# Performance work log

Measured on AMD Instinct MI355X. Metric: run time of the kernel, lower is better.

## Reference

```python
import jax, jax.numpy as jnp
import numpy as np

DIM = 2048
NUM_EXPERTS = 64
K = 2
TEMPERATURE = 1.0


def setup_inputs() -> dict:
    key = jax.random.key(0)
    kx, kw, kb = jax.random.split(key, 3)
    x = jax.random.normal(kx, (4, 4096, DIM), dtype=jnp.float32)
    # nn.Linear(dim, num_experts): weight [num_experts, dim], bias [num_experts]
    bound = 1.0 / np.sqrt(DIM)
    W = jax.random.uniform(kw, (NUM_EXPERTS, DIM), dtype=jnp.float32, minval=-bound, maxval=bound)
    b = jax.random.uniform(kb, (NUM_EXPERTS,), dtype=jnp.float32, minval=-bound, maxval=bound)
    return {"x": x, "W": W, "b": b}


def reference(x, W, b):
    # logits: (batch, seq, num_experts)
    logits = (jnp.einsum('bsd,ed->bse', x, W) + b) / TEMPERATURE
    probs = jax.nn.softmax(logits, axis=-1)
    values, indices = jax.lax.top_k(probs, K)
    return indices, values
```

## Files before the change

### kernel.cpp

```cpp
#include <hip/hip_runtime.h>
#include <math.h>

typedef _Float16 half8 __attribute__((ext_vector_type(8)));
typedef float floatx16 __attribute__((ext_vector_type(16)));

#define DIMK 2048
#define NEXP 64
#define BM 32
#define KSPLIT 4
#define KPW (DIMK / KSPLIT)
#define CHUNK 64
#define NCHUNK (KPW / CHUNK)
#define KSTEP 16
#define NKS (CHUNK / KSTEP)

__global__ void SwitchRouter_wsplit(const float* __restrict__ W, _Float16* __restrict__ ws) {
    int t = blockIdx.x * 256 + threadIdx.x;
    if (t >= NEXP * DIMK) return;
    int e = t >> 11, k = t & (DIMK - 1);
    float w = W[e * DIMK + k];
    _Float16 h0 = (_Float16)w;
    _Float16 h1 = (_Float16)(w - (float)h0);
    int kb8 = k >> 3, kj = k & 7;
    ws[(((kb8 * 2 + 0) << 9) + (e << 3) + kj)] = h0;
    ws[(((kb8 * 2 + 1) << 9) + (e << 3) + kj)] = h1;
}

__device__ __forceinline__ bool gt_pair(float v, int i, float v2, int i2) {
    return (v > v2) || (v == v2 && i < i2);
}

__device__ __forceinline__ void stage_chunk(const float* xg, float* dst, int lane) {
#pragma unroll
    for (int j = 0; j < 8; ++j) {
        int rowj = j * 4 + (lane >> 4);
        const float* src = xg + (size_t)rowj * DIMK + (((lane & 15) ^ (rowj & 15)) << 2);
        __builtin_amdgcn_global_load_lds(
            (const __attribute__((address_space(1))) void*)src,
            (__attribute__((address_space(3))) void*)(dst + j * 256),
            16, 0, 0);
    }
}

__device__ __forceinline__ half8 ldw(const _Float16* wsp, int kglob0, int half_, int et, int limb, int row) {
    int kb8 = (kglob0 >> 3) + half_;
    return *(const half8*)(wsp + (((size_t)(kb8 * 2 + limb) << 9) + (((et << 5) + row) << 3)));
}

__global__ __launch_bounds__(256, 2)
void SwitchRouter_43078521979510_kernel(const float* __restrict__ x,
                                        const _Float16* __restrict__ wsp,
                                        const float* __restrict__ bias,
                                        float* __restrict__ out, int M)
{
    __shared__ float lds[16384];

    const int t = threadIdx.x;
    const int wv = t >> 6;
    const int lane = t & 63;
    const int row = lane & 31;
    const int half_ = lane >> 5;
    const int r0 = blockIdx.x * BM;
    const int kwb = wv * KPW;

    float* atile = lds + wv * (2 * 2048);
    const float* xg0 = x + (size_t)r0 * DIMK + kwb;

    floatx16 accP0 = {}, accQ0 = {}, accP1 = {}, accQ1 = {};
    half8 w0[4], w1[4];

    stage_chunk(xg0 + 0 * CHUNK, atile + 0 * 2048, lane);
    stage_chunk(xg0 + 1 * CHUNK, atile + 1 * 2048, lane);
    {
        int kg = kwb + 0;
        w0[0] = ldw(wsp, kg, half_, 0, 0, row);
        w0[1] = ldw(wsp, kg, half_, 0, 1, row);
        w0[2] = ldw(wsp, kg, half_, 1, 0, row);
        w0[3] = ldw(wsp, kg, half_, 1, 1, row);
    }

    for (int c = 0; c < NCHUNK; ++c) {
        if (c == NCHUNK - 1) {
            asm volatile("s_waitcnt vmcnt(4)" ::: "memory");
        } else {
            asm volatile("s_waitcnt vmcnt(12)" ::: "memory");
        }
        const float* buf = atile + (c & 1) * 2048;

#pragma unroll
        for (int ks = 0; ks < NKS; ++ks) {
            const bool last = (c == NCHUNK - 1) && (ks == NKS - 1);
            if (!last) {
                int kgn = (ks == NKS - 1) ? (kwb + (c + 1) * CHUNK)
                                          : (kwb + c * CHUNK + (ks + 1) * KSTEP);
                if ((ks & 1) == 0) {
                    w1[0] = ldw(wsp, kgn, half_, 0, 0, row);
                    w1[1] = ldw(wsp, kgn, half_, 0, 1, row);
                    w1[2] = ldw(wsp, kgn, half_, 1, 0, row);
                    w1[3] = ldw(wsp, kgn, half_, 1, 1, row);
                } else {
                    w0[0] = ldw(wsp, kgn, half_, 0, 0, row);
                    w0[1] = ldw(wsp, kgn, half_, 0, 1, row);
                    w0[2] = ldw(wsp, kgn, half_, 1, 0, row);
                    w0[3] = ldw(wsp, kgn, half_, 1, 1, row);
                }
            }

            int g = ks * 4 + half_ * 2;
            int s0 = g ^ (row & 15);
            int s1 = (g + 1) ^ (row & 15);
            float4 fa = *(const float4*)&buf[row * 64 + s0 * 4];
            float4 fb = *(const float4*)&buf[row * 64 + s1 * 4];
            float f[8] = {fa.x, fa.y, fa.z, fa.w, fb.x, fb.y, fb.z, fb.w};
            half8 a0, a1;
#pragma unroll
            for (int i = 0; i < 8; ++i) {
                _Float16 h = (_Float16)f[i];
                a0[i] = h;
                a1[i] = (_Float16)(f[i] - (float)h);
            }

            const half8* wb = ((ks & 1) == 0) ? w0 : w1;
            accP0 = __builtin_amdgcn_mfma_f32_32x32x16_f16(a0, wb[0], accP0, 0, 0, 0);
            accQ0 = __builtin_amdgcn_mfma_f32_32x32x16_f16(a0, wb[1], accQ0, 0, 0, 0);
            accP1 = __builtin_amdgcn_mfma_f32_32x32x16_f16(a0, wb[2], accP1, 0, 0, 0);
            accQ1 = __builtin_amdgcn_mfma_f32_32x32x16_f16(a0, wb[3], accQ1, 0, 0, 0);
            accP0 = __builtin_amdgcn_mfma_f32_32x32x16_f16(a1, wb[1], accP0, 0, 0, 0);
            accQ0 = __builtin_amdgcn_mfma_f32_32x32x16_f16(a1, wb[0], accQ0, 0, 0, 0);
            accP1 = __builtin_amdgcn_mfma_f32_32x32x16_f16(a1, wb[3], accP1, 0, 0, 0);
            accQ1 = __builtin_amdgcn_mfma_f32_32x32x16_f16(a1, wb[2], accQ1, 0, 0, 0);
        }

        asm volatile("s_waitcnt lgkmcnt(0)" ::: "memory");
        if (c + 2 < NCHUNK) stage_chunk(xg0 + (c + 2) * CHUNK, atile + (c & 1) * 2048, lane);
    }

    __syncthreads();
    float* red = lds;
#pragma unroll
    for (int s = 0; s < 16; ++s) {
        int rowD = (s & 3) + 8 * (s >> 2) + 4 * half_;
        red[wv * 2176 + rowD * 68 + 0 * 32 + row] = accP0[s] + accQ0[s];
        red[wv * 2176 + rowD * 68 + 1 * 32 + row] = accP1[s] + accQ1[s];
    }
    __syncthreads();

    {
        const int rr = t >> 3;
        const int g8 = t & 7;
        float l[8];
#pragma unroll
        for (int j = 0; j < 8; ++j) {
            float s = 0.f;
#pragma unroll
            for (int w = 0; w < 4; ++w) s += red[w * 2176 + rr * 68 + g8 * 8 + j];
            l[j] = s + bias[g8 * 8 + j];
        }

        float v0 = l[0];
        int   i0 = 8 * g8;
        float v1 = -INFINITY;
        int   i1 = -1;
#pragma unroll
        for (int j = 1; j < 8; ++j) {
            const float lv = l[j];
            const int   e  = 8 * g8 + j;
            if (lv > v0) { v1 = v0; i1 = i0; v0 = lv; i0 = e; }
            else if (lv > v1) { v1 = lv; i1 = e; }
        }
#pragma unroll
        for (int m = 1; m <= 4; m <<= 1) {
            const float ov0 = __shfl_xor(v0, m);
            const int   oi0 = __shfl_xor(i0, m);
            const float ov1 = __shfl_xor(v1, m);
            const int   oi1 = __shfl_xor(i1, m);
            if (gt_pair(ov0, oi0, v0, i0)) {
                if (gt_pair(v0, i0, ov1, oi1)) { v1 = v0; i1 = i0; }
                else                           { v1 = ov1; i1 = oi1; }
                v0 = ov0; i0 = oi0;
            } else if (gt_pair(ov0, oi0, v1, i1)) {
                v1 = ov0; i1 = oi0;
            }
        }
        float d = 0.f;
#pragma unroll
        for (int j = 0; j < 8; ++j) d += expf(l[j] - v0);
#pragma unroll
        for (int m = 1; m <= 4; m <<= 1) d += __shfl_xor(d, m);

        if (g8 == 0) {
            const int R = r0 + rr;
            out[2 * R]     = (float)i0;
            out[2 * R + 1] = (float)i1;
            out[2 * M + 2 * R]     = 1.f / d;
            out[2 * M + 2 * R + 1] = expf(v1 - v0) / d;
        }
    }
}

extern "C" void kernel_launch(void* const* d_in, const int* in_sizes, int n_in,
                              void* d_out, int out_size, void* d_ws, size_t ws_size,
                              hipStream_t stream) {
    const float* x  = (const float*)d_in[0];
    const float* W  = (const float*)d_in[1];
    const float* b  = (const float*)d_in[2];
    float* out = (float*)d_out;
    _Float16* ws = (_Float16*)d_ws;
    const int M = in_sizes[0] / DIMK;

    SwitchRouter_wsplit<<<(NEXP * DIMK + 255) / 256, 256, 0, stream>>>(W, ws);
    SwitchRouter_43078521979510_kernel<<<M / BM, 256, 0, stream>>>(x, ws, b, out, M);
}
```

Baseline: 37.30 us.

## Switch to 16x16x32 MFMA with direct register loads and smaller row tiles

Replaces the LDS-staged 32x32x16 MFMA pipeline with 16x16x32 MFMAs that take x straight from global memory into registers, using a four-deep register prefetch. The block tile drops to 16 rows and occupancy is raised to 4 blocks per SIMD. The split-fp16 product also drops the lo*lo term, so each step issues three MFMAs instead of four. The weight pre-split layout is rewritten to match the new MFMA operand order. The aim is to cut LDS staging traffic and MFMA count and to launch more blocks. The trade-off is more weight reloads per row, since each block now covers fewer rows, and a small accuracy change from the dropped cross term.

```diff
diff --git a/kernel.cpp b/kernel.cpp
--- a/kernel.cpp
+++ b/kernel.cpp
@@ -2,17 +2,14 @@
 #include <math.h>
 
 typedef _Float16 half8 __attribute__((ext_vector_type(8)));
-typedef float floatx16 __attribute__((ext_vector_type(16)));
+typedef float f32x4 __attribute__((ext_vector_type(4)));
 
 #define DIMK 2048
 #define NEXP 64
-#define BM 32
+#define BM 16
 #define KSPLIT 4
 #define KPW (DIMK / KSPLIT)
-#define CHUNK 64
-#define NCHUNK (KPW / CHUNK)
-#define KSTEP 16
-#define NKS (CHUNK / KSTEP)
+#define NKS (KPW / 32)
 
 __global__ void SwitchRouter_wsplit(const float* __restrict__ W, _Float16* __restrict__ ws) {
     int t = blockIdx.x * 256 + threadIdx.x;
@@ -21,139 +18,92 @@
     float w = W[e * DIMK + k];
     _Float16 h0 = (_Float16)w;
     _Float16 h1 = (_Float16)(w - (float)h0);
-    int kb8 = k >> 3, kj = k & 7;
-    ws[(((kb8 * 2 + 0) << 9) + (e << 3) + kj)] = h0;
-    ws[(((kb8 * 2 + 1) << 9) + (e << 3) + kj)] = h1;
+    int kb32 = k >> 5;
+    int lane = (((k >> 3) & 3) << 4) | (e & 15);
+    int et   = e >> 4;
+    size_t base = ((size_t)(kb32 * 2 + 0) * 4 + et) * 512 + lane * 8 + (k & 7);
+    ws[base]        = h0;
+    ws[base + 2048] = h1;
 }
 
 __device__ __forceinline__ bool gt_pair(float v, int i, float v2, int i2) {
     return (v > v2) || (v == v2 && i < i2);
 }
 
-__device__ __forceinline__ void stage_chunk(const float* xg, float* dst, int lane) {
-#pragma unroll
-    for (int j = 0; j < 8; ++j) {
-        int rowj = j * 4 + (lane >> 4);
-        const float* src = xg + (size_t)rowj * DIMK + (((lane & 15) ^ (rowj & 15)) << 2);
-        __builtin_amdgcn_global_load_lds(
-            (const __attribute__((address_space(1))) void*)src,
-            (__attribute__((address_space(3))) void*)(dst + j * 256),
-            16, 0, 0);
-    }
-}
-
-__device__ __forceinline__ half8 ldw(const _Float16* wsp, int kglob0, int half_, int et, int limb, int row) {
-    int kb8 = (kglob0 >> 3) + half_;
-    return *(const half8*)(wsp + (((size_t)(kb8 * 2 + limb) << 9) + (((et << 5) + row) << 3)));
-}
-
-__global__ __launch_bounds__(256, 2)
+__global__ __launch_bounds__(256, 4)
 void SwitchRouter_43078521979510_kernel(const float* __restrict__ x,
-                                        const _Float16* __restrict__ wsp,
+                                        const _Float16* __restrict__ ws,
                                         const float* __restrict__ bias,
                                         float* __restrict__ out, int M)
 {
-    __shared__ float lds[16384];
+    __shared__ float red[KSPLIT * BM * 68];
 
-    const int t = threadIdx.x;
-    const int wv = t >> 6;
+    const int t    = threadIdx.x;
+    const int wv   = t >> 6;
     const int lane = t & 63;
-    const int row = lane & 31;
-    const int half_ = lane >> 5;
-    const int r0 = blockIdx.x * BM;
-    const int kwb = wv * KPW;
+    const int r0   = blockIdx.x * BM;
 
-    float* atile = lds + wv * (2 * 2048);
-    const float* xg0 = x + (size_t)r0 * DIMK + kwb;
+    const float* xr = x + (size_t)(r0 + (lane & 15)) * DIMK + wv * KPW + ((lane >> 4) << 3);
+    const _Float16* wp = ws + (size_t)(wv * NKS) * 4096 + lane * 8;
 
-    floatx16 accP0 = {}, accQ0 = {}, accP1 = {}, accQ1 = {};
-    half8 w0[4], w1[4];
+    f32x4 acc[4] = {};
 
-    stage_chunk(xg0 + 0 * CHUNK, atile + 0 * 2048, lane);
-    stage_chunk(xg0 + 1 * CHUNK, atile + 1 * 2048, lane);
-    {
-        int kg = kwb + 0;
-        w0[0] = ldw(wsp, kg, half_, 0, 0, row);
-        w0[1] = ldw(wsp, kg, half_, 0, 1, row);
-        w0[2] = ldw(wsp, kg, half_, 1, 0, row);
-        w0[3] = ldw(wsp, kg, half_, 1, 1, row);
+    float4 fa[4], fb[4];
+#pragma unroll
+    for (int d = 0; d < 4; ++d) {
+        fa[d] = *(const float4*)(xr + d * 32);
+        fb[d] = *(const float4*)(xr + d * 32 + 4);
     }
 
-    for (int c = 0; c < NCHUNK; ++c) {
-        if (c == NCHUNK - 1) {
-            asm volatile("s_waitcnt vmcnt(4)" ::: "memory");
-        } else {
-            asm volatile("s_waitcnt vmcnt(12)" ::: "memory");
+#pragma unroll
+    for (int ks = 0; ks < NKS; ++ks) {
+        half8 w[8];
+#pragma unroll
+        for (int q = 0; q < 8; ++q)
+            w[q] = *(const half8*)(wp + (size_t)ks * 4096 + q * 512);
+
+        const float4 va = fa[ks & 3], vb = fb[ks & 3];
+        const float f[8] = {va.x, va.y, va.z, va.w, vb.x, vb.y, vb.z, vb.w};
+        half8 a0, a1;
+#pragma unroll
+        for (int i = 0; i < 8; ++i) {
+            _Float16 h = (_Float16)f[i];
+            a0[i] = h;
+            a1[i] = (_Float16)(f[i] - (float)h);
         }
-        const float* buf = atile + (c & 1) * 2048;
 
 #pragma unroll
-        for (int ks = 0; ks < NKS; ++ks) {
-            const bool last = (c == NCHUNK - 1) && (ks == NKS - 1);
-            if (!last) {
-                int kgn = (ks == NKS - 1) ? (kwb + (c + 1) * CHUNK)
-                                          : (kwb + c * CHUNK + (ks + 1) * KSTEP);
-                if ((ks & 1) == 0) {
-                    w1[0] = ldw(wsp, kgn, half_, 0, 0, row);
-                    w1[1] = ldw(wsp, kgn, half_, 0, 1, row);
-                    w1[2] = ldw(wsp, kgn, half_, 1, 0, row);
-                    w1[3] = ldw(wsp, kgn, half_, 1, 1, row);
-                } else {
-                    w0[0] = ldw(wsp, kgn, half_, 0, 0, row);
-                    w0[1] = ldw(wsp, kgn, half_, 0, 1, row);
-                    w0[2] = ldw(wsp, kgn, half_, 1, 0, row);
-                    w0[3] = ldw(wsp, kgn, half_, 1, 1, row);
-                }
-            }
-
-            int g = ks * 4 + half_ * 2;
-            int s0 = g ^ (row & 15);
-            int s1 = (g + 1) ^ (row & 15);
-            float4 fa = *(const float4*)&buf[row * 64 + s0 * 4];
-            float4 fb = *(const float4*)&buf[row * 64 + s1 * 4];
-            float f[8] = {fa.x, fa.y, fa.z, fa.w, fb.x, fb.y, fb.z, fb.w};
-            half8 a0, a1;
-#pragma unroll
-            for (int i = 0; i < 8; ++i) {
-                _Float16 h = (_Float16)f[i];
-                a0[i] = h;
-                a1[i] = (_Float16)(f[i] - (float)h);
-            }
-
-            const half8* wb = ((ks & 1) == 0) ? w0 : w1;
-            accP0 = __builtin_amdgcn_mfma_f32_32x32x16_f16(a0, wb[0], accP0, 0, 0, 0);
-            accQ0 = __builtin_amdgcn_mfma_f32_32x32x16_f16(a0, wb[1], accQ0, 0, 0, 0);
-            accP1 = __builtin_amdgcn_mfma_f32_32x32x16_f16(a0, wb[2], accP1, 0, 0, 0);
-            accQ1 = __builtin_amdgcn_mfma_f32_32x32x16_f16(a0, wb[3], accQ1, 0, 0, 0);
-            accP0 = __builtin_amdgcn_mfma_f32_32x32x16_f16(a1, wb[1], accP0, 0, 0, 0);
-            accQ0 = __builtin_amdgcn_mfma_f32_32x32x16_f16(a1, wb[0], accQ0, 0, 0, 0);
-            accP1 = __builtin_amdgcn_mfma_f32_32x32x16_f16(a1, wb[3], accP1, 0, 0, 0);
-            accQ1 = __builtin_amdgcn_mfma_f32_32x32x16_f16(a1, wb[2], accQ1, 0, 0, 0);
+        for (int et = 0; et < 4; ++et) {
+            acc[et] = __builtin_amdgcn_mfma_f32_16x16x32_f16(a0, w[et],     acc[et], 0, 0, 0);
+            acc[et] = __builtin_amdgcn_mfma_f32_16x16x32_f16(a1, w[et],     acc[et], 0, 0, 0);
+            acc[et] = __builtin_amdgcn_mfma_f32_16x16x32_f16(a0, w[4 + et], acc[et], 0, 0, 0);
         }
 
-        asm volatile("s_waitcnt lgkmcnt(0)" ::: "memory");
-        if (c + 2 < NCHUNK) stage_chunk(xg0 + (c + 2) * CHUNK, atile + (c & 1) * 2048, lane);
+        if (ks + 4 < NKS) {
+            fa[ks & 3] = *(const float4*)(xr + (ks + 4) * 32);
+            fb[ks & 3] = *(const float4*)(xr + (ks + 4) * 32 + 4);
+        }
     }
 
-    __syncthreads();
-    float* red = lds;
 #pragma unroll
-    for (int s = 0; s < 16; ++s) {
-        int rowD = (s & 3) + 8 * (s >> 2) + 4 * half_;
-        red[wv * 2176 + rowD * 68 + 0 * 32 + row] = accP0[s] + accQ0[s];
-        red[wv * 2176 + rowD * 68 + 1 * 32 + row] = accP1[s] + accQ1[s];
-    }
+    for (int et = 0; et < 4; ++et)
+#pragma unroll
+        for (int r = 0; r < 4; ++r) {
+            const int m = ((lane >> 4) << 2) + r;
+            const int e = (et << 4) + (lane & 15);
+            red[(wv * BM + m) * 68 + e] = acc[et][r];
+        }
     __syncthreads();
 
-    {
-        const int rr = t >> 3;
-        const int g8 = t & 7;
+    if (t < BM * 8) {
+        const int row = t >> 3;
+        const int g8  = t & 7;
         float l[8];
 #pragma unroll
         for (int j = 0; j < 8; ++j) {
             float s = 0.f;
 #pragma unroll
-            for (int w = 0; w < 4; ++w) s += red[w * 2176 + rr * 68 + g8 * 8 + j];
+            for (int w2 = 0; w2 < KSPLIT; ++w2) s += red[(w2 * BM + row) * 68 + g8 * 8 + j];
             l[j] = s + bias[g8 * 8 + j];
         }
 
@@ -189,7 +139,7 @@
         for (int m = 1; m <= 4; m <<= 1) d += __shfl_xor(d, m);
 
         if (g8 == 0) {
-            const int R = r0 + rr;
+            const int R = r0 + row;
             out[2 * R]     = (float)i0;
             out[2 * R + 1] = (float)i1;
             out[2 * M + 2 * R]     = 1.f / d;
```

New measurement: 45.40 us. +21.7%, slower.

## Drop low-low split term, deepen weight prefetch, hoist LDS reads before restaging

Applied to the files above, without the earlier changes.

Cuts the split-fp16 product from four MFMAs per expert tile to three by dropping the lo*lo term, which shrinks matrix-core work by a quarter at a small accuracy cost. It also merges the accumulators into two chains, prefetches weight fragments three steps ahead through a four-slot ring, and reads the whole LDS chunk into registers before issuing the next async stage. The goal is to cut MFMA issue time and hide global and LDS latency, at the cost of more registers and serial dependent MFMA chains on each accumulator.

```diff
diff --git a/kernel.cpp b/kernel.cpp
--- a/kernel.cpp
+++ b/kernel.cpp
@@ -2,17 +2,18 @@
 #include <math.h>
 
 typedef _Float16 half8 __attribute__((ext_vector_type(8)));
-typedef float floatx16 __attribute__((ext_vector_type(16)));
+typedef float f32x16 __attribute__((ext_vector_type(16)));
 
 #define DIMK 2048
 #define NEXP 64
 #define BM 32
-#define KSPLIT 4
-#define KPW (DIMK / KSPLIT)
+#define NW 4
+#define KPW (DIMK / NW)
 #define CHUNK 64
 #define NCHUNK (KPW / CHUNK)
 #define KSTEP 16
 #define NKS (CHUNK / KSTEP)
+#define NU (NCHUNK * NKS)
 
 __global__ void SwitchRouter_wsplit(const float* __restrict__ W, _Float16* __restrict__ ws) {
     int t = blockIdx.x * 256 + threadIdx.x;
@@ -30,18 +31,6 @@
     return (v > v2) || (v == v2 && i < i2);
 }
 
-__device__ __forceinline__ void stage_chunk(const float* xg, float* dst, int lane) {
-#pragma unroll
-    for (int j = 0; j < 8; ++j) {
-        int rowj = j * 4 + (lane >> 4);
-        const float* src = xg + (size_t)rowj * DIMK + (((lane & 15) ^ (rowj & 15)) << 2);
-        __builtin_amdgcn_global_load_lds(
-            (const __attribute__((address_space(1))) void*)src,
-            (__attribute__((address_space(3))) void*)(dst + j * 256),
-            16, 0, 0);
-    }
-}
-
 __device__ __forceinline__ half8 ldw(const _Float16* wsp, int kglob0, int half_, int et, int limb, int row) {
     int kb8 = (kglob0 >> 3) + half_;
     return *(const half8*)(wsp + (((size_t)(kb8 * 2 + limb) << 9) + (((et << 5) + row) << 3)));
@@ -55,93 +44,100 @@
 {
     __shared__ float lds[16384];
 
-    const int t = threadIdx.x;
-    const int wv = t >> 6;
-    const int lane = t & 63;
-    const int row = lane & 31;
+    const int t     = threadIdx.x;
+    const int wv    = t >> 6;
+    const int lane  = t & 63;
+    const int row   = lane & 31;
     const int half_ = lane >> 5;
-    const int r0 = blockIdx.x * BM;
-    const int kwb = wv * KPW;
-
-    float* atile = lds + wv * (2 * 2048);
+    const int r0    = blockIdx.x * BM;
+    const int kwb   = wv * KPW;
+
+    float* atile = lds + wv * 4096;
     const float* xg0 = x + (size_t)r0 * DIMK + kwb;
 
-    floatx16 accP0 = {}, accQ0 = {}, accP1 = {}, accQ1 = {};
-    half8 w0[4], w1[4];
-
-    stage_chunk(xg0 + 0 * CHUNK, atile + 0 * 2048, lane);
-    stage_chunk(xg0 + 1 * CHUNK, atile + 1 * 2048, lane);
-    {
-        int kg = kwb + 0;
-        w0[0] = ldw(wsp, kg, half_, 0, 0, row);
-        w0[1] = ldw(wsp, kg, half_, 0, 1, row);
-        w0[2] = ldw(wsp, kg, half_, 1, 0, row);
-        w0[3] = ldw(wsp, kg, half_, 1, 1, row);
-    }
+#define STAGE(c)                                                                   \
+    {                                                                              \
+        float* dst = atile + ((c) & 1) * 2048;                                     \
+        _Pragma("unroll") for (int j = 0; j < 8; ++j) {                            \
+            const int rowj = j * 4 + (lane >> 4);                                  \
+            const float* src = xg0 + (size_t)rowj * DIMK + (c) * CHUNK             \
+                               + (((lane & 15) ^ (rowj & 15)) << 2);               \
+            __builtin_amdgcn_global_load_lds(                                      \
+                (const __attribute__((address_space(1))) void*)src,                \
+                (__attribute__((address_space(3))) void*)(dst + j * 256),          \
+                16, 0, 0);                                                         \
+        }                                                                          \
+    }
+
+#define LOADW(u, slot)                                                             \
+    {                                                                              \
+        const int kg = kwb + (u) * KSTEP;                                          \
+        wr[slot][0] = ldw(wsp, kg, half_, 0, 0, row);                              \
+        wr[slot][1] = ldw(wsp, kg, half_, 0, 1, row);                              \
+        wr[slot][2] = ldw(wsp, kg, half_, 1, 0, row);                              \
+        wr[slot][3] = ldw(wsp, kg, half_, 1, 1, row);                              \
+    }
+
+    half8 wr[4][4];
+    f32x16 acc[2] = {};
+
+    LOADW(0, 0);
+    LOADW(1, 1);
+    LOADW(2, 2);
+    STAGE(0);
+    STAGE(1);
 
     for (int c = 0; c < NCHUNK; ++c) {
-        if (c == NCHUNK - 1) {
-            asm volatile("s_waitcnt vmcnt(4)" ::: "memory");
-        } else {
-            asm volatile("s_waitcnt vmcnt(12)" ::: "memory");
-        }
+        if (c == 0)              { asm volatile("s_waitcnt vmcnt(8)"  ::: "memory"); }
+        else if (c == NCHUNK-1) { asm volatile("s_waitcnt vmcnt(0)"  ::: "memory"); }
+        else                     { asm volatile("s_waitcnt vmcnt(20)" ::: "memory"); }
+
         const float* buf = atile + (c & 1) * 2048;
 
+        float4 fA[NKS], fB[NKS];
 #pragma unroll
         for (int ks = 0; ks < NKS; ++ks) {
-            const bool last = (c == NCHUNK - 1) && (ks == NKS - 1);
-            if (!last) {
-                int kgn = (ks == NKS - 1) ? (kwb + (c + 1) * CHUNK)
-                                          : (kwb + c * CHUNK + (ks + 1) * KSTEP);
-                if ((ks & 1) == 0) {
-                    w1[0] = ldw(wsp, kgn, half_, 0, 0, row);
-                    w1[1] = ldw(wsp, kgn, half_, 0, 1, row);
-                    w1[2] = ldw(wsp, kgn, half_, 1, 0, row);
-                    w1[3] = ldw(wsp, kgn, half_, 1, 1, row);
-                } else {
-                    w0[0] = ldw(wsp, kgn, half_, 0, 0, row);
-                    w0[1] = ldw(wsp, kgn, half_, 0, 1, row);
-                    w0[2] = ldw(wsp, kgn, half_, 1, 0, row);
-                    w0[3] = ldw(wsp, kgn, half_, 1, 1, row);
-                }
+            const int g  = ks * 4 + half_ * 2;
+            const int s0 = g ^ (row & 15);
+            const int s1 = (g + 1) ^ (row & 15);
+            fA[ks] = *(const float4*)&buf[row * 64 + s0 * 4];
+            fB[ks] = *(const float4*)&buf[row * 64 + s1 * 4];
+        }
+        asm volatile("s_waitcnt lgkmcnt(0)" ::: "memory");
+        if (c + 2 < NCHUNK) STAGE(c + 2);
+
+#pragma unroll
+        for (int ks = 0; ks < NKS; ++ks) {
+            const int u = c * NKS + ks;
+            if (u + 3 < NU) LOADW(u + 3, (ks + 3) & 3);
+
+            const float4 va = fA[ks], vb = fB[ks];
+            const float f[8] = {va.x, va.y, va.z, va.w, vb.x, vb.y, vb.z, vb.w};
+            half8 a0, a1;
+#pragma unroll
+            for (int j = 0; j < 8; ++j) {
+                _Float16 h = (_Float16)f[j];
+                a0[j] = h;
+                a1[j] = (_Float16)(f[j] - (float)h);
             }
 
-            int g = ks * 4 + half_ * 2;
-            int s0 = g ^ (row & 15);
-            int s1 = (g + 1) ^ (row & 15);
-            float4 fa = *(const float4*)&buf[row * 64 + s0 * 4];
-            float4 fb = *(const float4*)&buf[row * 64 + s1 * 4];
-            float f[8] = {fa.x, fa.y, fa.z, fa.w, fb.x, fb.y, fb.z, fb.w};
-            half8 a0, a1;
-#pragma unroll
-            for (int i = 0; i < 8; ++i) {
-                _Float16 h = (_Float16)f[i];
-                a0[i] = h;
-                a1[i] = (_Float16)(f[i] - (float)h);
-            }
-
-            const half8* wb = ((ks & 1) == 0) ? w0 : w1;
-            accP0 = __builtin_amdgcn_mfma_f32_32x32x16_f16(a0, wb[0], accP0, 0, 0, 0);
-            accQ0 = __builtin_amdgcn_mfma_f32_32x32x16_f16(a0, wb[1], accQ0, 0, 0, 0);
-            accP1 = __builtin_amdgcn_mfma_f32_32x32x16_f16(a0, wb[2], accP1, 0, 0, 0);
-            accQ1 = __builtin_amdgcn_mfma_f32_32x32x16_f16(a0, wb[3], accQ1, 0, 0, 0);
-            accP0 = __builtin_amdgcn_mfma_f32_32x32x16_f16(a1, wb[1], accP0, 0, 0, 0);
-            accQ0 = __builtin_amdgcn_mfma_f32_32x32x16_f16(a1, wb[0], accQ0, 0, 0, 0);
-            accP1 = __builtin_amdgcn_mfma_f32_32x32x16_f16(a1, wb[3], accP1, 0, 0, 0);
-            accQ1 = __builtin_amdgcn_mfma_f32_32x32x16_f16(a1, wb[2], accQ1, 0, 0, 0);
-        }
-
-        asm volatile("s_waitcnt lgkmcnt(0)" ::: "memory");
-        if (c + 2 < NCHUNK) stage_chunk(xg0 + (c + 2) * CHUNK, atile + (c & 1) * 2048, lane);
+            const half8* w = wr[ks];
+            acc[0] = __builtin_amdgcn_mfma_f32_32x32x16_f16(a0, w[0], acc[0], 0, 0, 0);
+            acc[0] = __builtin_amdgcn_mfma_f32_32x32x16_f16(a1, w[0], acc[0], 0, 0, 0);
+            acc[0] = __builtin_amdgcn_mfma_f32_32x32x16_f16(a0, w[1], acc[0], 0, 0, 0);
+            acc[1] = __builtin_amdgcn_mfma_f32_32x32x16_f16(a0, w[2], acc[1], 0, 0, 0);
+            acc[1] = __builtin_amdgcn_mfma_f32_32x32x16_f16(a1, w[2], acc[1], 0, 0, 0);
+            acc[1] = __builtin_amdgcn_mfma_f32_32x32x16_f16(a0, w[3], acc[1], 0, 0, 0);
+        }
     }
 
     __syncthreads();
     float* red = lds;
 #pragma unroll
     for (int s = 0; s < 16; ++s) {
-        int rowD = (s & 3) + 8 * (s >> 2) + 4 * half_;
-        red[wv * 2176 + rowD * 68 + 0 * 32 + row] = accP0[s] + accQ0[s];
-        red[wv * 2176 + rowD * 68 + 1 * 32 + row] = accP1[s] + accQ1[s];
+        const int rowD = (s & 3) + 8 * (s >> 2) + 4 * half_;
+        red[wv * 2176 + rowD * 68 + 0 * 32 + row] = acc[0][s];
+        red[wv * 2176 + rowD * 68 + 1 * 32 + row] = acc[1][s];
     }
     __syncthreads();
 
@@ -153,7 +149,7 @@
         for (int j = 0; j < 8; ++j) {
             float s = 0.f;
 #pragma unroll
-            for (int w = 0; w < 4; ++w) s += red[w * 2176 + rr * 68 + g8 * 8 + j];
+            for (int w2 = 0; w2 < NW; ++w2) s += red[w2 * 2176 + rr * 68 + g8 * 8 + j];
             l[j] = s + bias[g8 * 8 + j];
         }
 
@@ -169,11 +165,11 @@
             else if (lv > v1) { v1 = lv; i1 = e; }
         }
 #pragma unroll
-        for (int m = 1; m <= 4; m <<= 1) {
-            const float ov0 = __shfl_xor(v0, m);
-            const int   oi0 = __shfl_xor(i0, m);
-            const float ov1 = __shfl_xor(v1, m);
-            const int   oi1 = __shfl_xor(i1, m);
+        for (int m2 = 1; m2 <= 4; m2 <<= 1) {
+            const float ov0 = __shfl_xor(v0, m2);
+            const int   oi0 = __shfl_xor(i0, m2);
+            const float ov1 = __shfl_xor(v1, m2);
+            const int   oi1 = __shfl_xor(i1, m2);
             if (gt_pair(ov0, oi0, v0, i0)) {
                 if (gt_pair(v0, i0, ov1, oi1)) { v1 = v0; i1 = i0; }
                 else                           { v1 = ov1; i1 = oi1; }
@@ -186,7 +182,7 @@
 #pragma unroll
         for (int j = 0; j < 8; ++j) d += expf(l[j] - v0);
 #pragma unroll
-        for (int m = 1; m <= 4; m <<= 1) d += __shfl_xor(d, m);
+        for (int m2 = 1; m2 <= 4; m2 <<= 1) d += __shfl_xor(d, m2);
 
         if (g8 == 0) {
             const int R = r0 + rr;
```

Result: no change. 36.78 us (-1.4%).
